# Performance work log

Hardware: AMD Instinct MI355X
Metric: run time of the kernel (lower is better)

The kernel has to match this reference:

```python
import jax, jax.numpy as jnp
import numpy as np

B, N, C = 8, 4096, 1024
H = 16
D = C // H  # head_dim = 64
SCALE = D ** -0.5


def setup_inputs() -> dict:
    key = jax.random.key(0)
    ks = jax.random.split(key, 5)
    s = 0.02
    return {
        "x": jax.random.normal(ks[0], (B, N, C), dtype=jnp.float32),
        "Wq": jax.random.normal(ks[1], (C, C), dtype=jnp.float32) * s,
        "Wk": jax.random.normal(ks[2], (C, C), dtype=jnp.float32) * s,
        "Wv": jax.random.normal(ks[3], (C, C), dtype=jnp.float32) * s,
        "Wp": jax.random.normal(ks[4], (C, C), dtype=jnp.float32) * s,
        "bp": jnp.zeros((C,), dtype=jnp.float32),
    }


def reference(x, Wq, Wk, Wv, Wp, bp):
    b, n, c = x.shape
    # nn.Linear: y = x @ W^T (no bias for q/k/v)
    def split_heads(y):
        # (B,N,C) -> (B,N,H,D) -> permute(0,2,3,1) -> (B,H,D,N)
        return jnp.transpose(y.reshape(b, n, H, D), (0, 2, 3, 1))

    q = split_heads(x @ Wq.T)  # (B,H,D,N)
    k = split_heads(x @ Wk.T)  # (B,H,D,N)
    v = split_heads(x @ Wv.T)  # (B,H,D,N)

    # attn over head_dim (faithful to source layout): (B,H,D,D)
    attn = jnp.einsum('bhdn,bhen->bhde', q, k) * SCALE
    attn = jax.nn.softmax(attn, axis=-1)
    # (B,H,D,D) @ (B,H,D,N) -> (B,H,D,N); transpose(1,2) -> (B,D,H,N); reshape (B,N,C)
    out = jnp.einsum('bhde,bhen->bhdn', attn, v)
    out = jnp.transpose(out, (0, 2, 1, 3)).reshape(b, n, c)
    return out @ Wp.T + bp
```

## Files before the change

### kernel.cpp

```cpp
#include <hip/hip_runtime.h>


typedef __attribute__((ext_vector_type(4))) float f32x4;
typedef __attribute__((ext_vector_type(8))) _Float16 f16x8;
typedef __attribute__((ext_vector_type(4))) unsigned short u16x4;

__device__ __forceinline__ unsigned short f2h(float f) {
  union { _Float16 h; unsigned short u; } v;
  v.h = (_Float16)f;
  return v.u;
}

__global__ void cvt_f32_f16(const float* __restrict__ in, unsigned short* __restrict__ out, int n) {
  int i = (blockIdx.x * blockDim.x + threadIdx.x) * 4;
  if (i >= n) return;
  float4 v = *(const float4*)(in + i);
  u16x4 o;
  o.x = f2h(v.x); o.y = f2h(v.y); o.z = f2h(v.z); o.w = f2h(v.w);
  *(u16x4*)(out + i) = o;
}

__global__ void cvt4_f32_f16(const float* __restrict__ s0, const float* __restrict__ s1,
                             const float* __restrict__ s2, const float* __restrict__ s3,
                             unsigned short* __restrict__ d0, unsigned short* __restrict__ d1,
                             unsigned short* __restrict__ d2, unsigned short* __restrict__ d3) {
  const float* src; unsigned short* dst;
  switch (blockIdx.y) {
    case 0: src = s0; dst = d0; break;
    case 1: src = s1; dst = d1; break;
    case 2: src = s2; dst = d2; break;
    default: src = s3; dst = d3; break;
  }
  int i = (blockIdx.x * blockDim.x + threadIdx.x) * 4;
  float4 v = *(const float4*)(src + i);
  u16x4 o;
  o.x = f2h(v.x); o.y = f2h(v.y); o.z = f2h(v.z); o.w = f2h(v.w);
  *(u16x4*)(dst + i) = o;
}

#define LDS_LD 68
enum { EPI_QKV = 0, EPI_F32_BIAS = 2 };

template <int EPI>
__global__ __launch_bounds__(256, 2) void gemm_bt(const unsigned short* __restrict__ A,
                                                  const unsigned short* __restrict__ Bt,
                                                  void* __restrict__ Cv,
                                                  const float* __restrict__ bias,
                                                  const int M, const int N, const int K) {
  __shared__ unsigned short lds[4 * 64 * LDS_LD];
  const int tid = threadIdx.x;
  const int wave = tid >> 6, lane = tid & 63;
  const int quad = lane >> 4, l15 = lane & 15;
  const int m0 = blockIdx.y * 128, n0 = blockIdx.x * 128;
  const int mb = (wave & 1) * 64, nb = (wave >> 1) * 64;

  const int sr = lane >> 2;
  const int sc = (lane & 3) ^ ((sr >> 1) & 3);

  const int swz = quad ^ ((l15 >> 1) & 3);
  int a_off[4], b_off[4];
#pragma unroll
  for (int t = 0; t < 4; t++) {
    a_off[t] = ((mb >> 4) + t) * 512 + (l15 * 4 + swz) * 8;
    b_off[t] = 4096 + ((nb >> 4) + t) * 512 + (l15 * 4 + swz) * 8;
  }

  const unsigned short* Ag = A + (size_t)(m0 + sr) * K + sc * 8;
  const unsigned short* Bg = Bt + (size_t)(n0 + sr) * K + sc * 8;

  f32x4 acc[4][4];
#pragma unroll
  for (int i = 0; i < 4; i++)
#pragma unroll
    for (int j = 0; j < 4; j++) acc[i][j] = f32x4{0.f, 0.f, 0.f, 0.f};

  for (int k0 = 0; k0 < K; k0 += 32) {
    __syncthreads();
#pragma unroll
    for (int rd = 0; rd < 2; rd++) {
      const int ch = rd * 4 + wave;
      __builtin_amdgcn_global_load_lds(
          (const __attribute__((address_space(1))) void*)(Ag + (size_t)ch * 16 * K + k0),
          (__attribute__((address_space(3))) void*)&lds[ch * 512], 16, 0, 0);
      __builtin_amdgcn_global_load_lds(
          (const __attribute__((address_space(1))) void*)(Bg + (size_t)ch * 16 * K + k0),
          (__attribute__((address_space(3))) void*)&lds[4096 + ch * 512], 16, 0, 0);
    }
    __syncthreads();

    f16x8 af[4], bf[4];
#pragma unroll
    for (int t = 0; t < 4; t++) {
      af[t] = *(const f16x8*)&lds[a_off[t]];
      bf[t] = *(const f16x8*)&lds[b_off[t]];
    }
#pragma unroll
    for (int mi = 0; mi < 4; mi++)
#pragma unroll
      for (int ni = 0; ni < 4; ni++)
        acc[mi][ni] = __builtin_amdgcn_mfma_f32_16x16x32_f16(af[mi], bf[ni], acc[mi][ni], 0, 0, 0);
  }

  __syncthreads();

  if (EPI == EPI_F32_BIAS) {
    float* C = (float*)Cv;
#pragma unroll
    for (int ni = 0; ni < 4; ni++) {
      const int col = n0 + nb + ni * 16 + l15;
      const float bv = bias[col];
#pragma unroll
      for (int mi = 0; mi < 4; mi++)
#pragma unroll
        for (int rr = 0; rr < 4; rr++) {
          const int row = m0 + mb + mi * 16 + quad * 4 + rr;
          C[(size_t)row * N + col] = acc[mi][ni][rr] + bv;
        }
    }
  } else {
    unsigned short* C = (unsigned short*)Cv;
    const bool isT = (n0 < 2048);
    unsigned short* w = &lds[wave * 64 * LDS_LD];
#pragma unroll
    for (int mi = 0; mi < 4; mi++)
#pragma unroll
      for (int ni = 0; ni < 4; ni++)
#pragma unroll
        for (int rr = 0; rr < 4; rr++) {
          const int rl = mi * 16 + quad * 4 + rr;
          const int cl = ni * 16 + l15;
          if (isT)
            w[cl * LDS_LD + rl] = f2h(acc[mi][ni][rr]);
          else
            w[rl * LDS_LD + cl] = f2h(acc[mi][ni][rr]);
        }
#pragma unroll
    for (int p = 0; p < 8; p++) {
      const int a = p * 8 + (lane >> 3);
      const int b8 = (lane & 7) * 8;
      u16x4 lo = *(const u16x4*)&w[a * LDS_LD + b8];
      u16x4 hi = *(const u16x4*)&w[a * LDS_LD + b8 + 4];
      size_t gi;
      if (isT)
        gi = (size_t)(n0 + nb + a) * M + (m0 + mb + b8);
      else
        gi = (size_t)2048 * 32768 + (size_t)(m0 + mb + a) * 1024 + (n0 - 2048 + nb + b8);
      *(u16x4*)&C[gi] = lo;
      *(u16x4*)&C[gi + 4] = hi;
    }
  }
}

__global__ __launch_bounds__(256) void attn_logits(const unsigned short* __restrict__ qkt,
                                                   float* __restrict__ pbuf) {
  const int h = blockIdx.x, b = blockIdx.y, s = blockIdx.z;
  const int tid = threadIdx.x;
  const int wave = tid >> 6, lane = tid & 63;
  const int quad = lane >> 4, l15 = lane & 15;

  f32x4 acc[4];
#pragma unroll
  for (int t = 0; t < 4; t++) acc[t] = f32x4{0.f, 0.f, 0.f, 0.f};

  const unsigned short* qp =
      qkt + (size_t)(h * 64 + wave * 16 + l15) * 32768 + b * 4096 + s * 512 + quad * 8;
  const unsigned short* kp[4];
#pragma unroll
  for (int et = 0; et < 4; et++)
    kp[et] = qkt + (size_t)(1024 + h * 64 + et * 16 + l15) * 32768 + b * 4096 + s * 512 + quad * 8;

#pragma unroll 4
  for (int k0 = 0; k0 < 512; k0 += 32) {
    f16x8 aq = *(const f16x8*)(qp + k0);
#pragma unroll
    for (int et = 0; et < 4; et++) {
      f16x8 bk = *(const f16x8*)(kp[et] + k0);
      acc[et] = __builtin_amdgcn_mfma_f32_16x16x32_f16(aq, bk, acc[et], 0, 0, 0);
    }
  }

  float* pb = pbuf + ((size_t)(b * 16 + h) * 8 + s) * 4096;
#pragma unroll
  for (int et = 0; et < 4; et++)
#pragma unroll
    for (int rr = 0; rr < 4; rr++)
      pb[(wave * 16 + quad * 4 + rr) * 64 + et * 16 + l15] = acc[et][rr];
}

__global__ __launch_bounds__(256) void attn_softmax(const float* __restrict__ pbuf,
                                                    unsigned short* __restrict__ pP) {
  const int bh = blockIdx.x;
  const int tid = threadIdx.x;
  const int d = tid >> 2, q4 = tid & 3;
  const float* pb = pbuf + (size_t)bh * 32768 + d * 64 + q4 * 16;

  float v[16];
#pragma unroll
  for (int i = 0; i < 16; i++) v[i] = 0.f;
  for (int s = 0; s < 8; s++) {
#pragma unroll
    for (int e4 = 0; e4 < 4; e4++) {
      float4 t = *(const float4*)(pb + s * 4096 + e4 * 4);
      v[e4 * 4 + 0] += t.x; v[e4 * 4 + 1] += t.y;
      v[e4 * 4 + 2] += t.z; v[e4 * 4 + 3] += t.w;
    }
  }
#pragma unroll
  for (int i = 0; i < 16; i++) v[i] *= 0.125f;

  float m = v[0];
#pragma unroll
  for (int i = 1; i < 16; i++) m = fmaxf(m, v[i]);
  m = fmaxf(m, __shfl_xor(m, 1));
  m = fmaxf(m, __shfl_xor(m, 2));
  float sum = 0.f;
#pragma unroll
  for (int i = 0; i < 16; i++) {
    v[i] = __expf(v[i] - m);
    sum += v[i];
  }
  sum += __shfl_xor(sum, 1);
  sum += __shfl_xor(sum, 2);
  const float inv = 1.f / sum;

  unsigned short* pp = pP + (size_t)bh * 4096 + d * 64 + q4 * 16;
#pragma unroll
  for (int e4 = 0; e4 < 4; e4++) {
    u16x4 o;
    o.x = f2h(v[e4 * 4 + 0] * inv); o.y = f2h(v[e4 * 4 + 1] * inv);
    o.z = f2h(v[e4 * 4 + 2] * inv); o.w = f2h(v[e4 * 4 + 3] * inv);
    *(u16x4*)(pp + e4 * 4) = o;
  }
}

__global__ __launch_bounds__(256) void attn_pv(const unsigned short* __restrict__ pP,
                                               const unsigned short* __restrict__ vbuf,
                                               unsigned short* __restrict__ y) {
  const int h = blockIdx.x, b = blockIdx.y, s = blockIdx.z;
  const int tid = threadIdx.x;
  const int wave = tid >> 6, lane = tid & 63;
  const int quad = lane >> 4, l15 = lane & 15;
  const int bh = b * 16 + h;

  const unsigned short* pp = pP + (size_t)bh * 4096 + (wave * 16 + l15) * 64 + quad * 8;
  f16x8 pa0 = *(const f16x8*)(pp);
  f16x8 pa1 = *(const f16x8*)(pp + 32);

  const unsigned short* vb =
      vbuf + (size_t)(b * 4096 + s * 512 + l15) * 1024 + h * 64 + quad * 8;
  unsigned short* yb = y + (size_t)b * (4096 * 1024);

#pragma unroll 4
  for (int nt = 0; nt < 32; nt++) {
    const unsigned short* vp = vb + (size_t)nt * 16 * 1024;
    f16x8 v0 = *(const f16x8*)(vp);
    f16x8 v1 = *(const f16x8*)(vp + 32);
    f32x4 o = f32x4{0.f, 0.f, 0.f, 0.f};
    o = __builtin_amdgcn_mfma_f32_16x16x32_f16(pa0, v0, o, 0, 0, 0);
    o = __builtin_amdgcn_mfma_f32_16x16x32_f16(pa1, v1, o, 0, 0, 0);
    const int n = s * 512 + nt * 16 + l15;
    const int nhi = n >> 10, nlo = n & 1023;
#pragma unroll
    for (int rr = 0; rr < 4; rr++) {
      const int d = wave * 16 + quad * 4 + rr;
      yb[(size_t)(d * 64 + h * 4 + nhi) * 1024 + nlo] = f2h(o[rr]);
    }
  }
}

extern "C" void kernel_launch(void* const* d_in, const int* in_sizes, int n_in, void* d_out,
                              int out_size, void* d_ws, size_t ws_size, hipStream_t stream) {
  (void)in_sizes; (void)n_in; (void)out_size; (void)ws_size;
  const float* x = (const float*)d_in[0];
  const float* Wq = (const float*)d_in[1];
  const float* Wk = (const float*)d_in[2];
  const float* Wv = (const float*)d_in[3];
  const float* Wp = (const float*)d_in[4];
  const float* bp = (const float*)d_in[5];

  char* ws = (char*)d_ws;
  unsigned short* xb = (unsigned short*)(ws);
  float* pbuf = (float*)(ws);
  unsigned short* yb = xb;
  unsigned short* qkt = (unsigned short*)(ws + (size_t)67108864);
  unsigned short* pP = qkt;
  unsigned short* vbuf = (unsigned short*)(ws + (size_t)201326592);
  unsigned short* wqkv = (unsigned short*)(ws + (size_t)268435456);
  unsigned short* wp = (unsigned short*)(ws + (size_t)274726912);

  cvt_f32_f16<<<32768, 256, 0, stream>>>(x, xb, 33554432);
  cvt4_f32_f16<<<dim3(1024, 4), 256, 0, stream>>>(Wq, Wk, Wv, Wp, wqkv, wqkv + 1048576,
                                                  wqkv + 2097152, wp);

  gemm_bt<EPI_QKV><<<dim3(24, 256), 256, 0, stream>>>(xb, wqkv, qkt, nullptr, 32768, 3072, 1024);

  attn_logits<<<dim3(16, 8, 8), 256, 0, stream>>>(qkt, pbuf);
  attn_softmax<<<128, 256, 0, stream>>>(pbuf, pP);
  attn_pv<<<dim3(16, 8, 8), 256, 0, stream>>>(pP, vbuf, yb);

  gemm_bt<EPI_F32_BIAS><<<dim3(8, 256), 256, 0, stream>>>(yb, wp, (float*)d_out, bp, 32768, 1024, 1024);
}
```

Measured before the change: 697.1 us.

## Use 32x32x16 MFMA in GEMM, swizzle block order, split attention over more chunks

The GEMM now computes its 64x64 per-wave tile with 32x32x16 MFMA instructions in place of 16x16x32 ones. This uses fewer LDS fragment loads per FLOP, and the epilogue indexing and LDS swizzle offsets are adapted to match. Block indices are remapped so consecutive blocks walk across M tiles for a fixed N tile, which is meant to improve L2 reuse of the weight tiles. The attention logits and PV kernels split the sequence into 16 chunks instead of 8, doubling grid parallelism at the cost of a larger partial-logit buffer for softmax to reduce.

```diff
diff --git a/kernel.cpp b/kernel.cpp
--- a/kernel.cpp
+++ b/kernel.cpp
@@ -2,6 +2,7 @@
 
 
 typedef __attribute__((ext_vector_type(4))) float f32x4;
+typedef __attribute__((ext_vector_type(16))) float f32x16;
 typedef __attribute__((ext_vector_type(8))) _Float16 f16x8;
 typedef __attribute__((ext_vector_type(4))) unsigned short u16x4;
 
@@ -50,29 +51,39 @@
   __shared__ unsigned short lds[4 * 64 * LDS_LD];
   const int tid = threadIdx.x;
   const int wave = tid >> 6, lane = tid & 63;
-  const int quad = lane >> 4, l15 = lane & 15;
-  const int m0 = blockIdx.y * 128, n0 = blockIdx.x * 128;
+  const int l31 = lane & 31, hw = lane >> 5;
+
+  const int lin = blockIdx.y * gridDim.x + blockIdx.x;
+  const int g = lin & 255;
+  const int mt = (g & 7) * 32 + (g >> 3);
+  const int nt = lin >> 8;
+  const int m0 = mt * 128, n0 = nt * 128;
   const int mb = (wave & 1) * 64, nb = (wave >> 1) * 64;
 
   const int sr = lane >> 2;
   const int sc = (lane & 3) ^ ((sr >> 1) & 3);
 
-  const int swz = quad ^ ((l15 >> 1) & 3);
-  int a_off[4], b_off[4];
-#pragma unroll
-  for (int t = 0; t < 4; t++) {
-    a_off[t] = ((mb >> 4) + t) * 512 + (l15 * 4 + swz) * 8;
-    b_off[t] = 4096 + ((nb >> 4) + t) * 512 + (l15 * 4 + swz) * 8;
-  }
+  const int rloc = l31 & 15;
+  const int rbase = (l31 >> 4) * 512 + rloc * 32;
+  const int sx = (rloc >> 1) & 3;
+  int a_off[2][2], b_off[2][2];
+#pragma unroll
+  for (int t = 0; t < 2; t++)
+#pragma unroll
+    for (int ks = 0; ks < 2; ks++) {
+      const int slot = (ks * 2 + hw) ^ sx;
+      a_off[t][ks] = ((wave & 1) * 4 + t * 2) * 512 + rbase + slot * 8;
+      b_off[t][ks] = 4096 + ((wave >> 1) * 4 + t * 2) * 512 + rbase + slot * 8;
+    }
 
   const unsigned short* Ag = A + (size_t)(m0 + sr) * K + sc * 8;
   const unsigned short* Bg = Bt + (size_t)(n0 + sr) * K + sc * 8;
 
-  f32x4 acc[4][4];
-#pragma unroll
-  for (int i = 0; i < 4; i++)
-#pragma unroll
-    for (int j = 0; j < 4; j++) acc[i][j] = f32x4{0.f, 0.f, 0.f, 0.f};
+  f32x16 acc[2][2];
+#pragma unroll
+  for (int i = 0; i < 2; i++)
+#pragma unroll
+    for (int j = 0; j < 2; j++) acc[i][j] = (f32x16)0.f;
 
   for (int k0 = 0; k0 < K; k0 += 32) {
     __syncthreads();
@@ -88,17 +99,22 @@
     }
     __syncthreads();
 
-    f16x8 af[4], bf[4];
-#pragma unroll
-    for (int t = 0; t < 4; t++) {
-      af[t] = *(const f16x8*)&lds[a_off[t]];
-      bf[t] = *(const f16x8*)&lds[b_off[t]];
-    }
-#pragma unroll
-    for (int mi = 0; mi < 4; mi++)
-#pragma unroll
-      for (int ni = 0; ni < 4; ni++)
-        acc[mi][ni] = __builtin_amdgcn_mfma_f32_16x16x32_f16(af[mi], bf[ni], acc[mi][ni], 0, 0, 0);
+    f16x8 af[2][2], bf[2][2];
+#pragma unroll
+    for (int t = 0; t < 2; t++)
+#pragma unroll
+      for (int ks = 0; ks < 2; ks++) {
+        af[t][ks] = *(const f16x8*)&lds[a_off[t][ks]];
+        bf[t][ks] = *(const f16x8*)&lds[b_off[t][ks]];
+      }
+#pragma unroll
+    for (int ks = 0; ks < 2; ks++)
+#pragma unroll
+      for (int mi = 0; mi < 2; mi++)
+#pragma unroll
+        for (int ni = 0; ni < 2; ni++)
+          acc[mi][ni] =
+              __builtin_amdgcn_mfma_f32_32x32x16_f16(af[mi][ks], bf[ni][ks], acc[mi][ni], 0, 0, 0);
   }
 
   __syncthreads();
@@ -106,15 +122,15 @@
   if (EPI == EPI_F32_BIAS) {
     float* C = (float*)Cv;
 #pragma unroll
-    for (int ni = 0; ni < 4; ni++) {
-      const int col = n0 + nb + ni * 16 + l15;
+    for (int ni = 0; ni < 2; ni++) {
+      const int col = n0 + nb + ni * 32 + l31;
       const float bv = bias[col];
 #pragma unroll
-      for (int mi = 0; mi < 4; mi++)
-#pragma unroll
-        for (int rr = 0; rr < 4; rr++) {
-          const int row = m0 + mb + mi * 16 + quad * 4 + rr;
-          C[(size_t)row * N + col] = acc[mi][ni][rr] + bv;
+      for (int mi = 0; mi < 2; mi++)
+#pragma unroll
+        for (int reg = 0; reg < 16; reg++) {
+          const int row = m0 + mb + mi * 32 + (reg & 3) + 8 * (reg >> 2) + 4 * hw;
+          C[(size_t)row * N + col] = acc[mi][ni][reg] + bv;
         }
     }
   } else {
@@ -122,17 +138,17 @@
     const bool isT = (n0 < 2048);
     unsigned short* w = &lds[wave * 64 * LDS_LD];
 #pragma unroll
-    for (int mi = 0; mi < 4; mi++)
-#pragma unroll
-      for (int ni = 0; ni < 4; ni++)
-#pragma unroll
-        for (int rr = 0; rr < 4; rr++) {
-          const int rl = mi * 16 + quad * 4 + rr;
-          const int cl = ni * 16 + l15;
+    for (int mi = 0; mi < 2; mi++)
+#pragma unroll
+      for (int ni = 0; ni < 2; ni++)
+#pragma unroll
+        for (int reg = 0; reg < 16; reg++) {
+          const int rl = mi * 32 + (reg & 3) + 8 * (reg >> 2) + 4 * hw;
+          const int cl = ni * 32 + l31;
           if (isT)
-            w[cl * LDS_LD + rl] = f2h(acc[mi][ni][rr]);
+            w[cl * LDS_LD + rl] = f2h(acc[mi][ni][reg]);
           else
-            w[rl * LDS_LD + cl] = f2h(acc[mi][ni][rr]);
+            w[rl * LDS_LD + cl] = f2h(acc[mi][ni][reg]);
         }
 #pragma unroll
     for (int p = 0; p < 8; p++) {
@@ -163,14 +179,14 @@
   for (int t = 0; t < 4; t++) acc[t] = f32x4{0.f, 0.f, 0.f, 0.f};
 
   const unsigned short* qp =
-      qkt + (size_t)(h * 64 + wave * 16 + l15) * 32768 + b * 4096 + s * 512 + quad * 8;
+      qkt + (size_t)(h * 64 + wave * 16 + l15) * 32768 + b * 4096 + s * 256 + quad * 8;
   const unsigned short* kp[4];
 #pragma unroll
   for (int et = 0; et < 4; et++)
-    kp[et] = qkt + (size_t)(1024 + h * 64 + et * 16 + l15) * 32768 + b * 4096 + s * 512 + quad * 8;
-
-#pragma unroll 4
-  for (int k0 = 0; k0 < 512; k0 += 32) {
+    kp[et] = qkt + (size_t)(1024 + h * 64 + et * 16 + l15) * 32768 + b * 4096 + s * 256 + quad * 8;
+
+#pragma unroll 2
+  for (int k0 = 0; k0 < 256; k0 += 32) {
     f16x8 aq = *(const f16x8*)(qp + k0);
 #pragma unroll
     for (int et = 0; et < 4; et++) {
@@ -179,7 +195,7 @@
     }
   }
 
-  float* pb = pbuf + ((size_t)(b * 16 + h) * 8 + s) * 4096;
+  float* pb = pbuf + ((size_t)(b * 16 + h) * 16 + s) * 4096;
 #pragma unroll
   for (int et = 0; et < 4; et++)
 #pragma unroll
@@ -192,12 +208,12 @@
   const int bh = blockIdx.x;
   const int tid = threadIdx.x;
   const int d = tid >> 2, q4 = tid & 3;
-  const float* pb = pbuf + (size_t)bh * 32768 + d * 64 + q4 * 16;
+  const float* pb = pbuf + (size_t)bh * 65536 + d * 64 + q4 * 16;
 
   float v[16];
 #pragma unroll
   for (int i = 0; i < 16; i++) v[i] = 0.f;
-  for (int s = 0; s < 8; s++) {
+  for (int s = 0; s < 16; s++) {
 #pragma unroll
     for (int e4 = 0; e4 < 4; e4++) {
       float4 t = *(const float4*)(pb + s * 4096 + e4 * 4);
@@ -247,18 +263,18 @@
   f16x8 pa1 = *(const f16x8*)(pp + 32);
 
   const unsigned short* vb =
-      vbuf + (size_t)(b * 4096 + s * 512 + l15) * 1024 + h * 64 + quad * 8;
+      vbuf + (size_t)(b * 4096 + s * 256 + l15) * 1024 + h * 64 + quad * 8;
   unsigned short* yb = y + (size_t)b * (4096 * 1024);
 
 #pragma unroll 4
-  for (int nt = 0; nt < 32; nt++) {
+  for (int nt = 0; nt < 16; nt++) {
     const unsigned short* vp = vb + (size_t)nt * 16 * 1024;
     f16x8 v0 = *(const f16x8*)(vp);
     f16x8 v1 = *(const f16x8*)(vp + 32);
     f32x4 o = f32x4{0.f, 0.f, 0.f, 0.f};
     o = __builtin_amdgcn_mfma_f32_16x16x32_f16(pa0, v0, o, 0, 0, 0);
     o = __builtin_amdgcn_mfma_f32_16x16x32_f16(pa1, v1, o, 0, 0, 0);
-    const int n = s * 512 + nt * 16 + l15;
+    const int n = s * 256 + nt * 16 + l15;
     const int nhi = n >> 10, nlo = n & 1023;
 #pragma unroll
     for (int rr = 0; rr < 4; rr++) {
@@ -294,9 +310,9 @@
 
   gemm_bt<EPI_QKV><<<dim3(24, 256), 256, 0, stream>>>(xb, wqkv, qkt, nullptr, 32768, 3072, 1024);
 
-  attn_logits<<<dim3(16, 8, 8), 256, 0, stream>>>(qkt, pbuf);
+  attn_logits<<<dim3(16, 8, 16), 256, 0, stream>>>(qkt, pbuf);
   attn_softmax<<<128, 256, 0, stream>>>(pbuf, pP);
-  attn_pv<<<dim3(16, 8, 8), 256, 0, stream>>>(pP, vbuf, yb);
+  attn_pv<<<dim3(16, 8, 16), 256, 0, stream>>>(pP, vbuf, yb);
 
   gemm_bt<EPI_F32_BIAS><<<dim3(8, 256), 256, 0, stream>>>(yb, wp, (float*)d_out, bp, 32768, 1024, 1024);
 }
```

New measurement: 735.7 us. 5.5% more time.

## Split attention over 16 sequence chunks and stage PV output through LDS

Applied to the files above, without the earlier changes.

The attention kernels now split the sequence dimension into 16 chunks of 256 instead of 8 chunks of 512, doubling the grid of the logits and PV kernels. The softmax kernel is reorganised so each block handles 16 rows and sums 16 partials with 16-lane shuffles, over 512 blocks. The PV kernel writes its fp16 results into a padded shared-memory tile and then stores them as 16-byte vectors to contiguous global rows, replacing scattered 2-byte stores. In exchange it doubles the partial-logit buffer traffic and adds a barrier and LDS use to the PV kernel.

```diff
diff --git a/kernel.cpp b/kernel.cpp
--- a/kernel.cpp
+++ b/kernel.cpp
@@ -4,6 +4,7 @@
 typedef __attribute__((ext_vector_type(4))) float f32x4;
 typedef __attribute__((ext_vector_type(8))) _Float16 f16x8;
 typedef __attribute__((ext_vector_type(4))) unsigned short u16x4;
+typedef __attribute__((ext_vector_type(8))) unsigned short u16x8;
 
 __device__ __forceinline__ unsigned short f2h(float f) {
   union { _Float16 h; unsigned short u; } v;
@@ -163,14 +164,14 @@
   for (int t = 0; t < 4; t++) acc[t] = f32x4{0.f, 0.f, 0.f, 0.f};
 
   const unsigned short* qp =
-      qkt + (size_t)(h * 64 + wave * 16 + l15) * 32768 + b * 4096 + s * 512 + quad * 8;
+      qkt + (size_t)(h * 64 + wave * 16 + l15) * 32768 + b * 4096 + s * 256 + quad * 8;
   const unsigned short* kp[4];
 #pragma unroll
   for (int et = 0; et < 4; et++)
-    kp[et] = qkt + (size_t)(1024 + h * 64 + et * 16 + l15) * 32768 + b * 4096 + s * 512 + quad * 8;
-
-#pragma unroll 4
-  for (int k0 = 0; k0 < 512; k0 += 32) {
+    kp[et] = qkt + (size_t)(1024 + h * 64 + et * 16 + l15) * 32768 + b * 4096 + s * 256 + quad * 8;
+
+#pragma unroll 2
+  for (int k0 = 0; k0 < 256; k0 += 32) {
     f16x8 aq = *(const f16x8*)(qp + k0);
 #pragma unroll
     for (int et = 0; et < 4; et++) {
@@ -179,7 +180,7 @@
     }
   }
 
-  float* pb = pbuf + ((size_t)(b * 16 + h) * 8 + s) * 4096;
+  float* pb = pbuf + ((size_t)(b * 16 + h) * 16 + s) * 4096;
 #pragma unroll
   for (int et = 0; et < 4; et++)
 #pragma unroll
@@ -189,53 +190,42 @@
 
 __global__ __launch_bounds__(256) void attn_softmax(const float* __restrict__ pbuf,
                                                     unsigned short* __restrict__ pP) {
-  const int bh = blockIdx.x;
-  const int tid = threadIdx.x;
-  const int d = tid >> 2, q4 = tid & 3;
-  const float* pb = pbuf + (size_t)bh * 32768 + d * 64 + q4 * 16;
-
-  float v[16];
-#pragma unroll
-  for (int i = 0; i < 16; i++) v[i] = 0.f;
-  for (int s = 0; s < 8; s++) {
-#pragma unroll
-    for (int e4 = 0; e4 < 4; e4++) {
-      float4 t = *(const float4*)(pb + s * 4096 + e4 * 4);
-      v[e4 * 4 + 0] += t.x; v[e4 * 4 + 1] += t.y;
-      v[e4 * 4 + 2] += t.z; v[e4 * 4 + 3] += t.w;
-    }
-  }
-#pragma unroll
-  for (int i = 0; i < 16; i++) v[i] *= 0.125f;
-
-  float m = v[0];
-#pragma unroll
-  for (int i = 1; i < 16; i++) m = fmaxf(m, v[i]);
-  m = fmaxf(m, __shfl_xor(m, 1));
-  m = fmaxf(m, __shfl_xor(m, 2));
+  const int bh = blockIdx.x >> 2, dg = blockIdx.x & 3;
+  const int t = threadIdx.x;
+  const int d = dg * 16 + (t >> 4), e4 = t & 15;
+  const float* pb = pbuf + (size_t)bh * 65536 + d * 64 + e4 * 4;
+
+  float v[4] = {0.f, 0.f, 0.f, 0.f};
+  for (int s = 0; s < 16; s++) {
+    float4 tt = *(const float4*)(pb + s * 4096);
+    v[0] += tt.x; v[1] += tt.y; v[2] += tt.z; v[3] += tt.w;
+  }
+#pragma unroll
+  for (int i = 0; i < 4; i++) v[i] *= 0.125f;
+
+  float m = fmaxf(fmaxf(v[0], v[1]), fmaxf(v[2], v[3]));
+#pragma unroll
+  for (int o = 1; o < 16; o <<= 1) m = fmaxf(m, __shfl_xor(m, o, 16));
   float sum = 0.f;
 #pragma unroll
-  for (int i = 0; i < 16; i++) {
+  for (int i = 0; i < 4; i++) {
     v[i] = __expf(v[i] - m);
     sum += v[i];
   }
-  sum += __shfl_xor(sum, 1);
-  sum += __shfl_xor(sum, 2);
+#pragma unroll
+  for (int o = 1; o < 16; o <<= 1) sum += __shfl_xor(sum, o, 16);
   const float inv = 1.f / sum;
 
-  unsigned short* pp = pP + (size_t)bh * 4096 + d * 64 + q4 * 16;
-#pragma unroll
-  for (int e4 = 0; e4 < 4; e4++) {
-    u16x4 o;
-    o.x = f2h(v[e4 * 4 + 0] * inv); o.y = f2h(v[e4 * 4 + 1] * inv);
-    o.z = f2h(v[e4 * 4 + 2] * inv); o.w = f2h(v[e4 * 4 + 3] * inv);
-    *(u16x4*)(pp + e4 * 4) = o;
-  }
+  u16x4 o4;
+  o4.x = f2h(v[0] * inv); o4.y = f2h(v[1] * inv);
+  o4.z = f2h(v[2] * inv); o4.w = f2h(v[3] * inv);
+  *(u16x4*)(pP + (size_t)bh * 4096 + d * 64 + e4 * 4) = o4;
 }
 
 __global__ __launch_bounds__(256) void attn_pv(const unsigned short* __restrict__ pP,
                                                const unsigned short* __restrict__ vbuf,
                                                unsigned short* __restrict__ y) {
+  __shared__ unsigned short tile[64 * 264];
   const int h = blockIdx.x, b = blockIdx.y, s = blockIdx.z;
   const int tid = threadIdx.x;
   const int wave = tid >> 6, lane = tid & 63;
@@ -247,25 +237,31 @@
   f16x8 pa1 = *(const f16x8*)(pp + 32);
 
   const unsigned short* vb =
-      vbuf + (size_t)(b * 4096 + s * 512 + l15) * 1024 + h * 64 + quad * 8;
-  unsigned short* yb = y + (size_t)b * (4096 * 1024);
+      vbuf + (size_t)(b * 4096 + s * 256 + l15) * 1024 + h * 64 + quad * 8;
 
 #pragma unroll 4
-  for (int nt = 0; nt < 32; nt++) {
+  for (int nt = 0; nt < 16; nt++) {
     const unsigned short* vp = vb + (size_t)nt * 16 * 1024;
     f16x8 v0 = *(const f16x8*)(vp);
     f16x8 v1 = *(const f16x8*)(vp + 32);
     f32x4 o = f32x4{0.f, 0.f, 0.f, 0.f};
     o = __builtin_amdgcn_mfma_f32_16x16x32_f16(pa0, v0, o, 0, 0, 0);
     o = __builtin_amdgcn_mfma_f32_16x16x32_f16(pa1, v1, o, 0, 0, 0);
-    const int n = s * 512 + nt * 16 + l15;
-    const int nhi = n >> 10, nlo = n & 1023;
-#pragma unroll
-    for (int rr = 0; rr < 4; rr++) {
-      const int d = wave * 16 + quad * 4 + rr;
-      yb[(size_t)(d * 64 + h * 4 + nhi) * 1024 + nlo] = f2h(o[rr]);
-    }
-  }
+    const int ncol = nt * 16 + l15;
+#pragma unroll
+    for (int rr = 0; rr < 4; rr++)
+      tile[(wave * 16 + quad * 4 + rr) * 264 + ncol] = f2h(o[rr]);
+  }
+  __syncthreads();
+
+  const int d = tid & 63, cc = tid >> 6;
+  const int R = d * 64 + h * 4 + (s >> 2);
+  unsigned short* dst =
+      y + (size_t)b * 4194304 + (size_t)R * 1024 + (s & 3) * 256 + cc * 64;
+  const unsigned short* srcp = &tile[d * 264 + cc * 64];
+#pragma unroll
+  for (int i = 0; i < 8; i++)
+    *(u16x8*)(dst + i * 8) = *(const u16x8*)(srcp + i * 8);
 }
 
 extern "C" void kernel_launch(void* const* d_in, const int* in_sizes, int n_in, void* d_out,
@@ -294,9 +290,9 @@
 
   gemm_bt<EPI_QKV><<<dim3(24, 256), 256, 0, stream>>>(xb, wqkv, qkt, nullptr, 32768, 3072, 1024);
 
-  attn_logits<<<dim3(16, 8, 8), 256, 0, stream>>>(qkt, pbuf);
-  attn_softmax<<<128, 256, 0, stream>>>(pbuf, pP);
-  attn_pv<<<dim3(16, 8, 8), 256, 0, stream>>>(pP, vbuf, yb);
+  attn_logits<<<dim3(16, 8, 16), 256, 0, stream>>>(qkt, pbuf);
+  attn_softmax<<<512, 256, 0, stream>>>(pbuf, pP);
+  attn_pv<<<dim3(16, 8, 16), 256, 0, stream>>>(pP, vbuf, yb);
 
   gemm_bt<EPI_F32_BIAS><<<dim3(8, 256), 256, 0, stream>>>(yb, wp, (float*)d_out, bp, 32768, 1024, 1024);
 }
```

New measurement: 693.3 us. No clear change (-0.6%).
